# Kernel optimization log

Hardware: AMD Instinct MI355X
Metric: run time of the kernel (lower is better)

## Reference

```python
import jax, jax.numpy as jnp
import numpy as np

# dims derived from config (hidden=512, d_state=64, d_conv=4, expand=2, headdim=64, ngroups=1)
D_MODEL = 512
D_STATE = 64
D_CONV = 4
D_INNER = 2 * D_MODEL          # 1024
HEADDIM = 64
NHEADS = D_INNER // HEADDIM    # 16
CONV_DIM = D_INNER + 2 * D_STATE   # 1152
D_IN_PROJ = 2 * D_INNER + 2 * D_STATE + NHEADS  # 2192
B = 4
L_TOT = 1024                   # seq_len (1008) + puzzle_emb_len (16)
INTER_T = 2816                 # find_multiple(round(4*1024*2/3), 256)
INTER_M = 1536                 # find_multiple(round(4*512*2/3), 256)
EPS = 1e-5


def rms_norm(x, eps=EPS):
    # weightless RMSNorm computed in fp32 (as HRM's rms_norm)
    x32 = x.astype(jnp.float32)
    y = x32 * jax.lax.rsqrt(jnp.mean(x32 * x32, axis=-1, keepdims=True) + eps)
    return y.astype(x.dtype)


def silu(x):
    return x * jax.nn.sigmoid(x)


def swiglu(x, w_gu, w_d):
    gate, up = jnp.split(x @ w_gu.T, 2, axis=-1)
    return (silu(gate) * up) @ w_d.T


def mamba2(u, in_proj_w, conv_w, conv_b, dt_bias, A_log, D, norm_w, out_proj_w):
    b, l, _ = u.shape
    zxbcdt = u @ in_proj_w.T                       # (b, l, D_IN_PROJ)
    z = zxbcdt[..., :D_INNER]
    xBC = zxbcdt[..., D_INNER:D_INNER + CONV_DIM]
    dt = jax.nn.softplus(zxbcdt[..., -NHEADS:] + dt_bias)  # (b, l, H)
    # causal depthwise conv1d over time + SiLU
    xp = jnp.pad(xBC, ((0, 0), (D_CONV - 1, 0), (0, 0)))
    xc = conv_b + sum(xp[:, i:i + l, :] * conv_w[:, i] for i in range(D_CONV))
    xBC = silu(xc)
    x = xBC[..., :D_INNER].reshape(b, l, NHEADS, HEADDIM)      # (b,l,h,p)
    Bm = xBC[..., D_INNER:D_INNER + D_STATE]                    # (b,l,n) ngroups=1
    Cm = xBC[..., D_INNER + D_STATE:]                           # (b,l,n)
    A = -jnp.exp(A_log)                                         # (h,)

    def step(s, inp):
        x_t, B_t, C_t, dt_t = inp                # (b,h,p) (b,n) (b,n) (b,h)
        dA = jnp.exp(dt_t * A)                   # (b,h)
        s = s * dA[:, :, None, None] + (dt_t[:, :, None] * x_t)[..., None] * B_t[:, None, None, :]
        y_t = jnp.einsum('bhpn,bn->bhp', s, C_t)
        return s, y_t

    s0 = jnp.zeros((b, NHEADS, HEADDIM, D_STATE), u.dtype)
    xs = (x.transpose(1, 0, 2, 3), Bm.transpose(1, 0, 2), Cm.transpose(1, 0, 2), dt.transpose(1, 0, 2))
    _, ys = jax.lax.scan(step, s0, xs)
    y = ys.transpose(1, 0, 2, 3) + x * D[None, None, :, None]   # skip term D*x per head
    y = y.reshape(b, l, D_INNER)
    # gated RMSNorm (norm_before_gate=False): norm(y * silu(z)) * weight
    g = y * silu(z)
    g32 = g.astype(jnp.float32)
    g = (g32 * jax.lax.rsqrt(jnp.mean(g32 * g32, axis=-1, keepdims=True) + EPS)).astype(g.dtype) * norm_w
    return g @ out_proj_w.T


def setup_inputs() -> dict:
    key = jax.random.key(0)
    ks = jax.random.split(key, 12)
    s = 0.02
    return {
        'hidden_states': jax.random.normal(ks[0], (B, L_TOT, D_MODEL), jnp.float32),
        'in_proj_w': jax.random.normal(ks[1], (D_IN_PROJ, D_MODEL), jnp.float32) * s,
        'conv_w': jax.random.normal(ks[2], (CONV_DIM, D_CONV), jnp.float32) * 0.1,
        'conv_b': jnp.zeros((CONV_DIM,), jnp.float32),
        'dt_bias': jax.random.normal(ks[3], (NHEADS,), jnp.float32) * 0.5,
        'A_log': jnp.log(jnp.arange(1, NHEADS + 1, dtype=jnp.float32)),
        'D': jnp.ones((NHEADS,), jnp.float32),
        'norm_w': jnp.ones((D_INNER,), jnp.float32),
        'out_proj_w': jax.random.normal(ks[4], (D_MODEL, D_INNER), jnp.float32) * s,
        'gu_t': jax.random.normal(ks[5], (2 * INTER_T, L_TOT), jnp.float32) * s,
        'down_t': jax.random.normal(ks[6], (L_TOT, INTER_T), jnp.float32) * s,
        'gu_m': jax.random.normal(ks[7], (2 * INTER_M, D_MODEL), jnp.float32) * s,
        'down_m': jax.random.normal(ks[8], (D_MODEL, INTER_M), jnp.float32) * s,
    }


def reference(hidden_states, in_proj_w, conv_w, conv_b, dt_bias, A_log, D, norm_w, out_proj_w, gu_t, down_t, gu_m, down_m):
    # Mamba2 mixer -> post-norm
    h = rms_norm(hidden_states + mamba2(hidden_states, in_proj_w, conv_w, conv_b, dt_bias, A_log, D, norm_w, out_proj_w))
    # MLP-t cross mixer over the sequence dim -> post-norm
    x = h.transpose(0, 2, 1)                 # (b, d, L)
    x = rms_norm(x + swiglu(x, gu_t, down_t))
    h = x.transpose(0, 2, 1)
    # token MLP -> post-norm
    h = rms_norm(h + swiglu(h, gu_m, down_m))
    return h
```

## Files before the change

### kernel.cpp

```cpp
#include <hip/hip_runtime.h>


#define BB 4
#define LL 1024
#define DMODEL 512
#define DINNER 1024
#define NHEADS 16
#define HEADDIM 64
#define DSTATE 64
#define CONVDIM 1152
#define NPROJ 2192
#define NPROJ_PAD 2304
#define INTER_T 2816
#define INTER_M 1536
#define NCHUNK 32
#define CHUNK 32

typedef __bf16 bf16x8 __attribute__((ext_vector_type(8)));
typedef float  f32x4  __attribute__((ext_vector_type(4)));
typedef unsigned short u16;
typedef unsigned int   u32;
typedef unsigned short u16x8 __attribute__((ext_vector_type(8)));

__device__ __forceinline__ u16 f2bf(float x) {
    union { float f; u32 u; } v; v.f = x;
    u32 u = v.u;
    return (u16)((u + 0x7fffu + ((u >> 16) & 1u)) >> 16);
}
__device__ __forceinline__ float silu_f(float x) {
    return x / (1.f + __expf(-x));
}
__device__ __forceinline__ float bf2f(u16 w) {
    union { u32 u; float f; } a; a.u = ((u32)w) << 16; return a.f;
}

__device__ __forceinline__ void cstore(float* p, float v) { *p = v; }
__device__ __forceinline__ void cstore(u16*   p, float v) { *p = f2bf(v); }

__device__ __forceinline__ void gld_lds16(const u16* g, u16* l) {
    __builtin_amdgcn_global_load_lds(
        (const __attribute__((address_space(1))) unsigned int*)g,
        (__attribute__((address_space(3))) unsigned int*)l, 16, 0, 0);
}

__device__ __forceinline__ float block_sum(float v) {
    #pragma unroll
    for (int off = 32; off > 0; off >>= 1) v += __shfl_xor(v, off, 64);
    __shared__ float red[4];
    int w = threadIdx.x >> 6;
    int nwv = blockDim.x >> 6;
    if ((threadIdx.x & 63) == 0) red[w] = v;
    __syncthreads();
    float tot = red[0];
    for (int i = 1; i < nwv; i++) tot += red[i];
    return tot;
}

#define HID_E      2097152LL
#define INPROJ_P_E 1179648LL
#define INPROJ_S_E 1122304LL
#define OUTPROJ_E   524288LL
#define GUT_E      5767168LL
#define DOWNT_E    2883584LL
#define GUM_E      1572864LL
#define DOWNM_E     786432LL
#define CONV_TOT_E 14811136LL

__global__ __launch_bounds__(256) void convert_all_kernel(
    const float* __restrict__ s_hid, const float* __restrict__ s_inproj,
    const float* __restrict__ s_outproj, const float* __restrict__ s_gut,
    const float* __restrict__ s_downt, const float* __restrict__ s_gum,
    const float* __restrict__ s_downm, u16* __restrict__ dst)
{
    long long idx = (long long)blockIdx.x * 256 + threadIdx.x;
    long long e = idx * 4;
    if (e >= CONV_TOT_E) return;
    const float* src; long long off, nsrc;
    long long c0 = HID_E;
    long long c1 = c0 + INPROJ_P_E;
    long long c2 = c1 + OUTPROJ_E;
    long long c3 = c2 + GUT_E;
    long long c4 = c3 + DOWNT_E;
    long long c5 = c4 + GUM_E;
    if      (e < c0) { src = s_hid;     off = e;      nsrc = HID_E; }
    else if (e < c1) { src = s_inproj;  off = e - c0; nsrc = INPROJ_S_E; }
    else if (e < c2) { src = s_outproj; off = e - c1; nsrc = OUTPROJ_E; }
    else if (e < c3) { src = s_gut;     off = e - c2; nsrc = GUT_E; }
    else if (e < c4) { src = s_downt;   off = e - c3; nsrc = DOWNT_E; }
    else if (e < c5) { src = s_gum;     off = e - c4; nsrc = GUM_E; }
    else             { src = s_downm;   off = e - c5; nsrc = DOWNM_E; }
    ushort4 r;
    if (off < nsrc) {
        float4 v = *reinterpret_cast<const float4*>(src + off);
        r.x = f2bf(v.x); r.y = f2bf(v.y); r.z = f2bf(v.z); r.w = f2bf(v.w);
    } else {
        r.x = 0; r.y = 0; r.z = 0; r.w = 0;
    }
    *reinterpret_cast<ushort4*>(dst + e) = r;
}

template<bool SK, typename CT>
__device__ __forceinline__ void gemm_bt_body(
    const u16* __restrict__ A, const u16* __restrict__ W,
    CT* __restrict__ C, int M, int N, int K, int kLen)
{
    __shared__ u16 As[128 * 64];
    __shared__ u16 Bs[128 * 64];
    int tid = threadIdx.x;
    int m0 = blockIdx.y * 128, n0 = blockIdx.x * 128;
    int kBase = SK ? blockIdx.z * kLen : 0;
    CT* Cw = SK ? C + (size_t)blockIdx.z * M * N : C;
    int wave = tid >> 6, lane = tid & 63;
    int wm = (wave >> 1) * 64, wn = (wave & 1) * 64;
    int lrow = lane & 15;
    int kq = lane >> 4;
    int kx = lrow & 7;

    int rL = lane >> 3, cL = lane & 7;
    int cG = cL ^ rL;
    const u16* gA[4]; const u16* gB[4];
    u16 *lA[4], *lB[4];
    #pragma unroll
    for (int i = 0; i < 4; i++) {
        int r = wave * 32 + i * 8;
        gA[i] = A + (size_t)(m0 + r + rL) * K + kBase + cG * 8;
        gB[i] = W + (size_t)(n0 + r + rL) * K + kBase + cG * 8;
        lA[i] = &As[r * 64];
        lB[i] = &Bs[r * 64];
    }

    f32x4 acc[4][4];
    #pragma unroll
    for (int i = 0; i < 4; i++)
        #pragma unroll
        for (int j = 0; j < 4; j++) {
            acc[i][j][0] = 0.f; acc[i][j][1] = 0.f;
            acc[i][j][2] = 0.f; acc[i][j][3] = 0.f;
        }

    for (int kt = 0; kt < kLen; kt += 64) {
        __syncthreads();
        #pragma unroll
        for (int i = 0; i < 4; i++) {
            gld_lds16(gA[i] + kt, lA[i]);
            gld_lds16(gB[i] + kt, lB[i]);
        }
        __syncthreads();
        #pragma unroll
        for (int ks = 0; ks < 2; ks++) {
            int ko = (((ks * 4 + kq) ^ kx) * 8);
            bf16x8 af[4], bfr[4];
            #pragma unroll
            for (int i = 0; i < 4; i++) {
                af[i]  = *reinterpret_cast<const bf16x8*>(&As[(wm + i * 16 + lrow) * 64 + ko]);
                bfr[i] = *reinterpret_cast<const bf16x8*>(&Bs[(wn + i * 16 + lrow) * 64 + ko]);
            }
            #pragma unroll
            for (int i = 0; i < 4; i++)
                #pragma unroll
                for (int j = 0; j < 4; j++)
                    acc[i][j] = __builtin_amdgcn_mfma_f32_16x16x32_bf16(af[i], bfr[j], acc[i][j], 0, 0, 0);
        }
    }

    int rbase = m0 + wm + kq * 4;
    int cbase = n0 + wn + lrow;
    #pragma unroll
    for (int i = 0; i < 4; i++)
        #pragma unroll
        for (int j = 0; j < 4; j++)
            #pragma unroll
            for (int r = 0; r < 4; r++)
                cstore(&Cw[(size_t)(rbase + i * 16 + r) * N + cbase + j * 16], acc[i][j][r]);
}

__global__ __launch_bounds__(256) void gemm_bt(
    const u16* __restrict__ A, const u16* __restrict__ W,
    u16* __restrict__ C, int M, int N, int K)
{
    gemm_bt_body<false, u16>(A, W, C, M, N, K, K);
}

__global__ __launch_bounds__(256) void gemm_bt_sk(
    const u16* __restrict__ A, const u16* __restrict__ W,
    u16* __restrict__ C, int M, int N, int K, int kLen)
{
    gemm_bt_body<true, u16>(A, W, C, M, N, K, kLen);
}

__global__ __launch_bounds__(256) void gemm_swiglu(
    const u16* __restrict__ A, const u16* __restrict__ W,
    u16* __restrict__ act, int M, int inter, int K)
{
    __shared__ u16 As[128 * 64];
    __shared__ u16 Bs[128 * 64];
    int tid = threadIdx.x;
    int m0 = blockIdx.y * 128, n0 = blockIdx.x * 64;
    int wave = tid >> 6, lane = tid & 63;
    int wm = (wave >> 1) * 64, wn = (wave & 1) * 32;
    int lrow = lane & 15;
    int kq = lane >> 4;
    int kx = lrow & 7;

    int rL = lane >> 3, cL = lane & 7;
    int cG = cL ^ rL;
    const u16* gA[4]; const u16* gB[4];
    u16 *lA[4], *lB[4];
    #pragma unroll
    for (int i = 0; i < 4; i++) {
        int r = wave * 32 + i * 8;
        gA[i] = A + (size_t)(m0 + r + rL) * K + cG * 8;
        lA[i] = &As[r * 64];
        int rB = r;
        int grow = (rB < 64) ? (n0 + rB + rL)
                             : (inter + n0 + rB - 64 + rL);
        gB[i] = W + (size_t)grow * K + cG * 8;
        lB[i] = &Bs[rB * 64];
    }

    f32x4 accg[4][2], accu[4][2];
    #pragma unroll
    for (int i = 0; i < 4; i++)
        #pragma unroll
        for (int j = 0; j < 2; j++) {
            accg[i][j][0]=0.f; accg[i][j][1]=0.f; accg[i][j][2]=0.f; accg[i][j][3]=0.f;
            accu[i][j][0]=0.f; accu[i][j][1]=0.f; accu[i][j][2]=0.f; accu[i][j][3]=0.f;
        }

    for (int kt = 0; kt < K; kt += 64) {
        __syncthreads();
        #pragma unroll
        for (int i = 0; i < 4; i++) {
            gld_lds16(gA[i] + kt, lA[i]);
            gld_lds16(gB[i] + kt, lB[i]);
        }
        __syncthreads();
        #pragma unroll
        for (int ks = 0; ks < 2; ks++) {
            int ko = (((ks * 4 + kq) ^ kx) * 8);
            bf16x8 af[4], bg[2], bu[2];
            #pragma unroll
            for (int i = 0; i < 4; i++)
                af[i] = *reinterpret_cast<const bf16x8*>(&As[(wm + i * 16 + lrow) * 64 + ko]);
            #pragma unroll
            for (int j = 0; j < 2; j++) {
                bg[j] = *reinterpret_cast<const bf16x8*>(&Bs[(wn + j * 16 + lrow) * 64 + ko]);
                bu[j] = *reinterpret_cast<const bf16x8*>(&Bs[(64 + wn + j * 16 + lrow) * 64 + ko]);
            }
            #pragma unroll
            for (int i = 0; i < 4; i++)
                #pragma unroll
                for (int j = 0; j < 2; j++) {
                    accg[i][j] = __builtin_amdgcn_mfma_f32_16x16x32_bf16(af[i], bg[j], accg[i][j], 0, 0, 0);
                    accu[i][j] = __builtin_amdgcn_mfma_f32_16x16x32_bf16(af[i], bu[j], accu[i][j], 0, 0, 0);
                }
        }
    }

    int rbase = m0 + wm + kq * 4;
    int cbase = n0 + wn + lrow;
    #pragma unroll
    for (int i = 0; i < 4; i++)
        #pragma unroll
        for (int j = 0; j < 2; j++)
            #pragma unroll
            for (int r = 0; r < 4; r++) {
                float g = accg[i][j][r], u = accu[i][j][r];
                act[(size_t)(rbase + i * 16 + r) * inter + cbase + j * 16] =
                    f2bf(silu_f(g) * u);
            }
}

__global__ __launch_bounds__(256) void conv_dt_kernel(
    const u16* __restrict__ zx, const float* __restrict__ conv_w,
    const float* __restrict__ conv_b, const float* __restrict__ dt_bias,
    u16* __restrict__ convout, float* __restrict__ dtbuf)
{
    int idx = blockIdx.x * 256 + threadIdx.x;
    int bl = idx / 1168;
    int c  = idx - bl * 1168;
    int l  = bl & (LL - 1);
    if (c < CONVDIM) {
        const u16* col = zx + (size_t)bl * NPROJ_PAD + DINNER + c;
        float acc = conv_b[c];
        #pragma unroll
        for (int i = 0; i < 4; i++) {
            int lt = l - 3 + i;
            float v = (lt >= 0) ? bf2f(col[(long long)(lt - l) * NPROJ_PAD]) : 0.f;
            acc = fmaf(v, conv_w[c * 4 + i], acc);
        }
        convout[(size_t)bl * CONVDIM + c] = f2bf(silu_f(acc));
    } else {
        int h = c - CONVDIM;
        float v = bf2f(zx[(size_t)bl * NPROJ_PAD + 2176 + h]) + dt_bias[h];
        float sp = (v > 20.f) ? v : log1pf(__expf(v));
        dtbuf[(size_t)bl * NHEADS + h] = sp;
    }
}

__global__ __launch_bounds__(256) void scan_mfma1(
    const u16* __restrict__ convout, const float* __restrict__ dtbuf,
    const float* __restrict__ A_log, u16* __restrict__ Sc,
    float* __restrict__ Ptot, u16* __restrict__ yp0)
{
    __shared__ u16 Blds[32 * 72];
    __shared__ u16 Clds[32 * 72];
    __shared__ u16 Xt[4][64 * 40];
    __shared__ u16 Bht[4][64 * 40];
    __shared__ u16 Wlds[4][32 * 40];
    __shared__ float dtl[4][32], cuml[4][32], warr[4][32];

    int blk = blockIdx.x;
    int c   = blk & 31;
    int bg  = blk >> 5;
    int b   = bg >> 2;
    int hq  = bg & 3;
    int tid = threadIdx.x;
    int w    = tid >> 6;
    int lane = tid & 63;
    int h   = hq * 4 + w;
    int bh  = b * 16 + h;
    int lrow = lane & 15, kq = lane >> 4;
    size_t base = ((size_t)b * LL + (size_t)c * CHUNK) * CONVDIM;
    float Ah = -__expf(A_log[h]);

    if (lane < 32)
        dtl[w][lane] = dtbuf[((size_t)b * LL + (size_t)c * CHUNK + lane) * NHEADS + h];
    #pragma unroll
    for (int it = 0; it < 2; ++it) {
        int idx = it * 256 + tid;
        int t = idx >> 4, q = idx & 15;
        u16x8 v = *reinterpret_cast<const u16x8*>(
            &convout[base + (size_t)t * CONVDIM + DINNER + q * 8]);
        if (q < 8) *reinterpret_cast<u16x8*>(&Blds[t * 72 + q * 8]) = v;
        else       *reinterpret_cast<u16x8*>(&Clds[t * 72 + (q - 8) * 8]) = v;
    }
    #pragma unroll
    for (int t = 0; t < 32; ++t)
        Xt[w][lane * 40 + t] = convout[base + (size_t)t * CONVDIM + h * HEADDIM + lane];
    __syncthreads();

    float s_inc = 0.f, s_all = 0.f;
    #pragma unroll
    for (int j = 0; j < 32; ++j) {
        float v = dtl[w][j];
        s_all += v;
        if (j <= lane) s_inc += v;
    }
    if (lane < 32) {
        cuml[w][lane] = s_inc;
        warr[w][lane] = __expf(Ah * (s_all - s_inc)) * dtl[w][lane];
    }
    float cumTot = s_all;
    __syncthreads();

    #pragma unroll
    for (int t = 0; t < 32; ++t)
        Bht[w][lane * 40 + t] = f2bf(warr[w][t] * bf2f(Blds[t * 72 + lane]));

    f32x4 accG[2][2];
    #pragma unroll
    for (int i = 0; i < 2; i++)
        #pragma unroll
        for (int j = 0; j < 2; j++) {
            accG[i][j][0]=0.f; accG[i][j][1]=0.f; accG[i][j][2]=0.f; accG[i][j][3]=0.f;
        }
    #pragma unroll
    for (int ks = 0; ks < 2; ++ks) {
        bf16x8 af[2], bfr[2];
        #pragma unroll
        for (int i = 0; i < 2; i++) {
            af[i]  = *reinterpret_cast<const bf16x8*>(&Clds[(16*i + lrow) * 72 + ks*32 + kq*8]);
            bfr[i] = *reinterpret_cast<const bf16x8*>(&Blds[(16*i + lrow) * 72 + ks*32 + kq*8]);
        }
        #pragma unroll
        for (int i = 0; i < 2; i++)
            #pragma unroll
            for (int j = 0; j < 2; j++)
                accG[i][j] = __builtin_amdgcn_mfma_f32_16x16x32_bf16(af[i], bfr[j], accG[i][j], 0, 0, 0);
    }

    float ctp0 = cuml[w][lrow],      dtp0 = dtl[w][lrow];
    float ctp1 = cuml[w][16 + lrow], dtp1 = dtl[w][16 + lrow];
    #pragma unroll
    for (int i = 0; i < 2; i++)
        #pragma unroll
        for (int r = 0; r < 4; r++) {
            int t = 16*i + kq*4 + r;
            float ct = cuml[w][t];
            #pragma unroll
            for (int j = 0; j < 2; j++) {
                int tp = 16*j + lrow;
                float ctp = j ? ctp1 : ctp0;
                float dtp = j ? dtp1 : dtp0;
                float g = accG[i][j][r];
                float wv = (tp <= t) ? __expf(Ah * (ct - ctp)) * dtp * g : 0.f;
                Wlds[w][t * 40 + tp] = f2bf(wv);
            }
        }
    __syncthreads();

    bf16x8 xf[4];
    #pragma unroll
    for (int j = 0; j < 4; j++)
        xf[j] = *reinterpret_cast<const bf16x8*>(&Xt[w][(16*j + lrow) * 40 + kq*8]);
    f32x4 accY[2][4];
    #pragma unroll
    for (int i = 0; i < 2; i++) {
        bf16x8 wf = *reinterpret_cast<const bf16x8*>(&Wlds[w][(16*i + lrow) * 40 + kq*8]);
        #pragma unroll
        for (int j = 0; j < 4; j++) {
            accY[i][j][0]=0.f; accY[i][j][1]=0.f; accY[i][j][2]=0.f; accY[i][j][3]=0.f;
            accY[i][j] = __builtin_amdgcn_mfma_f32_16x16x32_bf16(wf, xf[j], accY[i][j], 0, 0, 0);
        }
    }

    f32x4 accS[4][4];
    #pragma unroll
    for (int j = 0; j < 4; j++) {
        bf16x8 bb = *reinterpret_cast<const bf16x8*>(&Bht[w][(16*j + lrow) * 40 + kq*8]);
        #pragma unroll
        for (int i = 0; i < 4; i++) {
            accS[i][j][0]=0.f; accS[i][j][1]=0.f; accS[i][j][2]=0.f; accS[i][j][3]=0.f;
            accS[i][j] = __builtin_amdgcn_mfma_f32_16x16x32_bf16(xf[i], bb, accS[i][j], 0, 0, 0);
        }
    }

    u16* yb = yp0 + ((size_t)b * LL + (size_t)c * CHUNK) * DINNER + h * HEADDIM;
    #pragma unroll
    for (int i = 0; i < 2; i++)
        #pragma unroll
        for (int r = 0; r < 4; r++) {
            int t = 16*i + kq*4 + r;
            #pragma unroll
            for (int j = 0; j < 4; j++)
                yb[(size_t)t * DINNER + 16*j + lrow] = f2bf(accY[i][j][r]);
        }
    #pragma unroll
    for (int i = 0; i < 4; i++)
        #pragma unroll
        for (int r = 0; r < 4; r++) {
            int p = 16*i + kq*4 + r;
            #pragma unroll
            for (int j = 0; j < 4; j++)
                Sc[((size_t)(bh * 4 + j) * NCHUNK + c) * 1024 + p * 16 + lrow] = f2bf(accS[i][j][r]);
        }
    if (lane == 0) Ptot[bh * NCHUNK + c] = __expf(Ah * cumTot);
}

__global__ __launch_bounds__(256) void scan_combine(
    const u16* __restrict__ Sc, const float* __restrict__ Ptot,
    u16* __restrict__ Sinit)
{
    int blk = blockIdx.x;
    int bh = blk >> 2;
    int tid = threadIdx.x;
    int p = tid >> 2;
    int ncol = (tid & 3) * 4;
    float Pv[NCHUNK];
    #pragma unroll
    for (int c = 0; c < NCHUNK; ++c) Pv[c] = Ptot[bh * NCHUNK + c];
    float4 carry; carry.x = 0.f; carry.y = 0.f; carry.z = 0.f; carry.w = 0.f;
    size_t rowbase = (size_t)blk * NCHUNK * 1024 + p * 16 + ncol;
    #pragma unroll
    for (int c = 0; c < NCHUNK; ++c) {
        size_t row = rowbase + (size_t)c * 1024;
        ushort4 o;
        o.x = f2bf(carry.x); o.y = f2bf(carry.y);
        o.z = f2bf(carry.z); o.w = f2bf(carry.w);
        *reinterpret_cast<ushort4*>(Sinit + row) = o;
        ushort4 si = *reinterpret_cast<const ushort4*>(Sc + row);
        carry.x = fmaf(carry.x, Pv[c], bf2f(si.x));
        carry.y = fmaf(carry.y, Pv[c], bf2f(si.y));
        carry.z = fmaf(carry.z, Pv[c], bf2f(si.z));
        carry.w = fmaf(carry.w, Pv[c], bf2f(si.w));
    }
}

__global__ __launch_bounds__(256) void scan_mfma2(
    const u16* __restrict__ convout, const float* __restrict__ dtbuf,
    const float* __restrict__ A_log, const u16* __restrict__ Sinit,
    u16* __restrict__ yp1)
{
    __shared__ u16 Clds2[32 * 72];
    __shared__ float dtl[4][32], dacl[4][32];
    int blk = blockIdx.x;
    int c   = blk & 31;
    int bg  = blk >> 5;
    int b   = bg >> 2;
    int hq  = bg & 3;
    int tid = threadIdx.x;
    int w    = tid >> 6;
    int lane = tid & 63;
    int h   = hq * 4 + w;
    int bh  = b * 16 + h;
    int lrow = lane & 15, kq = lane >> 4;
    size_t base = ((size_t)b * LL + (size_t)c * CHUNK) * CONVDIM;
    float Ah = -__expf(A_log[h]);

    if (lane < 32)
        dtl[w][lane] = dtbuf[((size_t)b * LL + (size_t)c * CHUNK + lane) * NHEADS + h];
    {
        int t = tid >> 3, q = tid & 7;
        u16x8 v = *reinterpret_cast<const u16x8*>(
            &convout[base + (size_t)t * CONVDIM + DINNER + DSTATE + q * 8]);
        *reinterpret_cast<u16x8*>(&Clds2[t * 72 + q * 8]) = v;
    }
    __syncthreads();

    float s_inc = 0.f;
    #pragma unroll
    for (int j = 0; j < 32; ++j) {
        float v = dtl[w][j];
        if (j <= lane) s_inc += v;
    }
    if (lane < 32) dacl[w][lane] = __expf(Ah * s_inc);

    f32x4 accI[2][4];
    #pragma unroll
    for (int i = 0; i < 2; i++)
        #pragma unroll
        for (int j = 0; j < 4; j++) {
            accI[i][j][0]=0.f; accI[i][j][1]=0.f; accI[i][j][2]=0.f; accI[i][j][3]=0.f;
        }
    #pragma unroll
    for (int ks = 0; ks < 2; ++ks) {
        bf16x8 ca[2];
        #pragma unroll
        for (int i = 0; i < 2; i++)
            ca[i] = *reinterpret_cast<const bf16x8*>(&Clds2[(16*i + lrow) * 72 + ks*32 + kq*8]);
        int nq = ks * 2 + (kq >> 1);
        int off = (kq & 1) * 8;
        #pragma unroll
        for (int j = 0; j < 4; j++) {
            int p = 16*j + lrow;
            const u16* sp = Sinit + ((size_t)(bh * 4 + nq) * NCHUNK + c) * 1024 + p * 16 + off;
            bf16x8 fr = *reinterpret_cast<const bf16x8*>(sp);
            #pragma unroll
            for (int i = 0; i < 2; i++)
                accI[i][j] = __builtin_amdgcn_mfma_f32_16x16x32_bf16(ca[i], fr, accI[i][j], 0, 0, 0);
        }
    }

    u16* yb = yp1 + ((size_t)b * LL + (size_t)c * CHUNK) * DINNER + h * HEADDIM;
    #pragma unroll
    for (int i = 0; i < 2; i++)
        #pragma unroll
        for (int r = 0; r < 4; r++) {
            int t = 16*i + kq*4 + r;
            float sct = dacl[w][t];
            #pragma unroll
            for (int j = 0; j < 4; j++)
                yb[(size_t)t * DINNER + 16*j + lrow] = f2bf(accI[i][j][r] * sct);
        }
}

__global__ __launch_bounds__(256) void gated_rms_kernel(
    const u16* __restrict__ yp0, const u16* __restrict__ yp1,
    const u16* __restrict__ convout, const u16* __restrict__ zx,
    const float* __restrict__ Dv, const float* __restrict__ norm_w,
    u16* __restrict__ gout)
{
    int bl = blockIdx.x;
    int c = threadIdx.x * 4;
    ushort4 y0 = *reinterpret_cast<const ushort4*>(yp0 + (size_t)bl * DINNER + c);
    ushort4 y1 = *reinterpret_cast<const ushort4*>(yp1 + (size_t)bl * DINNER + c);
    ushort4 xv = *reinterpret_cast<const ushort4*>(convout + (size_t)bl * CONVDIM + c);
    ushort4 zv = *reinterpret_cast<const ushort4*>(zx + (size_t)bl * NPROJ_PAD + c);
    float Dh = Dv[c >> 6];
    float g0 = (bf2f(y0.x) + bf2f(y1.x) + bf2f(xv.x) * Dh) * silu_f(bf2f(zv.x));
    float g1 = (bf2f(y0.y) + bf2f(y1.y) + bf2f(xv.y) * Dh) * silu_f(bf2f(zv.y));
    float g2 = (bf2f(y0.z) + bf2f(y1.z) + bf2f(xv.z) * Dh) * silu_f(bf2f(zv.z));
    float g3 = (bf2f(y0.w) + bf2f(y1.w) + bf2f(xv.w) * Dh) * silu_f(bf2f(zv.w));
    float tot = block_sum(g0 * g0 + g1 * g1 + g2 * g2 + g3 * g3);
    float sc = rsqrtf(tot * (1.f / DINNER) + 1e-5f);
    float4 nw = *reinterpret_cast<const float4*>(norm_w + c);
    ushort4 o;
    o.x = f2bf(g0 * sc * nw.x); o.y = f2bf(g1 * sc * nw.y);
    o.z = f2bf(g2 * sc * nw.z); o.w = f2bf(g3 * sc * nw.w);
    *reinterpret_cast<ushort4*>(gout + (size_t)bl * DINNER + c) = o;
}

template<typename AT, typename OT>
__device__ __forceinline__ void residual_rms_body(
    const AT* __restrict__ a, const u16* __restrict__ pbuf,
    OT* __restrict__ outf, int ncols, int rows)
{
    int row = blockIdx.x;
    int c = threadIdx.x * 4;
    size_t slice = (size_t)rows * ncols;
    size_t off = (size_t)row * ncols + c;
    float va0, va1, va2, va3;
    if constexpr (sizeof(AT) == 4) {
        float4 t = *reinterpret_cast<const float4*>((const float*)a + off);
        va0 = t.x; va1 = t.y; va2 = t.z; va3 = t.w;
    } else {
        ushort4 t = *reinterpret_cast<const ushort4*>((const u16*)a + off);
        va0 = bf2f(t.x); va1 = bf2f(t.y); va2 = bf2f(t.z); va3 = bf2f(t.w);
    }
    ushort4 p0 = *reinterpret_cast<const ushort4*>(pbuf + off);
    ushort4 p1 = *reinterpret_cast<const ushort4*>(pbuf + slice + off);
    ushort4 p2 = *reinterpret_cast<const ushort4*>(pbuf + 2 * slice + off);
    ushort4 p3 = *reinterpret_cast<const ushort4*>(pbuf + 3 * slice + off);
    float v0 = va0 + ((bf2f(p0.x) + bf2f(p1.x)) + (bf2f(p2.x) + bf2f(p3.x)));
    float v1 = va1 + ((bf2f(p0.y) + bf2f(p1.y)) + (bf2f(p2.y) + bf2f(p3.y)));
    float v2 = va2 + ((bf2f(p0.z) + bf2f(p1.z)) + (bf2f(p2.z) + bf2f(p3.z)));
    float v3 = va3 + ((bf2f(p0.w) + bf2f(p1.w)) + (bf2f(p2.w) + bf2f(p3.w)));
    float tot = block_sum(v0 * v0 + v1 * v1 + v2 * v2 + v3 * v3);
    float sc = rsqrtf(tot / (float)ncols + 1e-5f);
    if constexpr (sizeof(OT) == 4) {
        float4 o; o.x = v0 * sc; o.y = v1 * sc; o.z = v2 * sc; o.w = v3 * sc;
        *reinterpret_cast<float4*>((float*)outf + off) = o;
    } else {
        ushort4 o;
        o.x = f2bf(v0 * sc); o.y = f2bf(v1 * sc);
        o.z = f2bf(v2 * sc); o.w = f2bf(v3 * sc);
        *reinterpret_cast<ushort4*>((u16*)outf + off) = o;
    }
}

__global__ void residual_rms_f2b(const float* __restrict__ a,
    const u16* __restrict__ pbuf, u16* __restrict__ o, int ncols, int rows)
{ residual_rms_body<float, u16>(a, pbuf, o, ncols, rows); }

__global__ void residual_rms_b2b(const u16* __restrict__ a,
    const u16* __restrict__ pbuf, u16* __restrict__ o, int ncols, int rows)
{ residual_rms_body<u16, u16>(a, pbuf, o, ncols, rows); }

__global__ void residual_rms_b2f(const u16* __restrict__ a,
    const u16* __restrict__ pbuf, float* __restrict__ o, int ncols, int rows)
{ residual_rms_body<u16, float>(a, pbuf, o, ncols, rows); }

__global__ __launch_bounds__(256) void transpose_bf16_kernel(
    const u16* __restrict__ in, u16* __restrict__ outb, int R, int C)
{
    __shared__ u16 tile[32][34];
    int b = blockIdx.z;
    int c0 = blockIdx.x * 32, r0 = blockIdx.y * 32;
    const u16* ip = in + (size_t)b * R * C;
    for (int i = threadIdx.y; i < 32; i += 8)
        tile[i][threadIdx.x] = ip[(size_t)(r0 + i) * C + c0 + threadIdx.x];
    __syncthreads();
    size_t ob = (size_t)b * R * C;
    for (int i = threadIdx.y; i < 32; i += 8)
        outb[ob + (size_t)(c0 + i) * R + r0 + threadIdx.x] = tile[threadIdx.x][i];
}

extern "C" void kernel_launch(void* const* d_in, const int* in_sizes, int n_in,
                              void* d_out, int out_size, void* d_ws, size_t ws_size,
                              hipStream_t stream)
{
    const float* hid      = (const float*)d_in[0];
    const float* in_proj  = (const float*)d_in[1];
    const float* conv_w   = (const float*)d_in[2];
    const float* conv_b   = (const float*)d_in[3];
    const float* dt_bias  = (const float*)d_in[4];
    const float* A_log    = (const float*)d_in[5];
    const float* Dv       = (const float*)d_in[6];
    const float* norm_w   = (const float*)d_in[7];
    const float* out_proj = (const float*)d_in[8];
    const float* gu_t     = (const float*)d_in[9];
    const float* down_t   = (const float*)d_in[10];
    const float* gu_m     = (const float*)d_in[11];
    const float* down_m   = (const float*)d_in[12];
    float* outp = (float*)d_out;

    char* ws = (char*)d_ws;
    u16* bf        = (u16*)ws;
    u16* hid_bf    = bf;
    u16* w_inproj  = bf + HID_E;
    u16* w_outproj = w_inproj + INPROJ_P_E;
    u16* w_gut     = w_outproj + OUTPROJ_E;
    u16* w_downt   = w_gut + GUT_E;
    u16* w_gum     = w_downt + DOWNT_E;
    u16* w_downm   = w_gum + GUM_E;
    size_t o = (size_t)(CONV_TOT_E * 2);
    auto alloc = [&](size_t bytes) { size_t r = o; o = (o + bytes + 255) & ~(size_t)255; return r; };
    size_t dt_off  = alloc(4096 * 16 * 4);
    size_t g_off   = alloc((size_t)4096 * 1024 * 2);
    size_t h1_off  = alloc((size_t)4096 * 512 * 4);
    size_t Pt_off  = alloc(2048 * 4);
    size_t xtb_off = alloc((size_t)2048 * 1024 * 2);
    size_t xtf_off = alloc((size_t)2048 * 1024 * 4);
    size_t act1_off= alloc((size_t)2048 * 2816 * 2);
    size_t x2_off  = alloc((size_t)2048 * 1024 * 4);
    size_t h2b_off = alloc((size_t)4096 * 512 * 2);
    size_t h2f_off = alloc((size_t)4096 * 512 * 4);
    size_t act2_off= alloc((size_t)4096 * 1536 * 2);
    size_t pad_off = alloc((size_t)10 * 1024 * 1024);
    size_t Sc_off  = xtb_off;
    size_t Si_off  = xtb_off + (size_t)8192 * 1024 * 4;
    (void)pad_off; (void)xtf_off; (void)h2f_off;
    size_t R_off   = o;
    size_t zx_off  = R_off;
    size_t cv_off  = zx_off + (size_t)4096 * NPROJ_PAD * 4;
    size_t y_off   = cv_off + (size_t)4096 * CONVDIM * 4;
    size_t sk_off  = R_off;

    u16*   zx      = (u16*)(ws + zx_off);
    u16*   convout = (u16*)(ws + cv_off);
    u16*   ybuf    = (u16*)(ws + y_off);
    float* dtbuf   = (float*)(ws + dt_off);
    u16*   g_bf    = (u16*)(ws + g_off);
    u16*   h1_bf   = (u16*)(ws + h1_off);
    u16*   xt_bf   = (u16*)(ws + xtb_off);
    u16*   act1    = (u16*)(ws + act1_off);
    u16*   x2_bf   = (u16*)(ws + x2_off);
    u16*   h2_bf   = (u16*)(ws + h2b_off);
    u16*   act2    = (u16*)(ws + act2_off);
    u16*   skbuf   = (u16*)(ws + sk_off);
    u16*   Sc      = (u16*)(ws + Sc_off);
    u16*   Sinit   = (u16*)(ws + Si_off);
    float* Ptot    = (float*)(ws + Pt_off);

    convert_all_kernel<<<14464, 256, 0, stream>>>(
        hid, in_proj, out_proj, gu_t, down_t, gu_m, down_m, bf);

    gemm_bt<<<dim3(NPROJ_PAD / 128, 4096 / 128), 256, 0, stream>>>(
        hid_bf, w_inproj, zx, 4096, NPROJ_PAD, 512);

    conv_dt_kernel<<<18688, 256, 0, stream>>>(zx, conv_w, conv_b, dt_bias, convout, dtbuf);

    scan_mfma1<<<512, 256, 0, stream>>>(convout, dtbuf, A_log, Sc, Ptot, ybuf);
    scan_combine<<<256, 256, 0, stream>>>(Sc, Ptot, Sinit);
    scan_mfma2<<<512, 256, 0, stream>>>(convout, dtbuf, A_log, Sinit, Sc);

    gated_rms_kernel<<<4096, 256, 0, stream>>>(ybuf, Sc, convout, zx, Dv, norm_w, g_bf);

    gemm_bt_sk<<<dim3(512 / 128, 4096 / 128, 4), 256, 0, stream>>>(
        g_bf, w_outproj, skbuf, 4096, 512, 1024, 256);

    residual_rms_f2b<<<4096, 128, 0, stream>>>(hid, skbuf, h1_bf, 512, 4096);

    transpose_bf16_kernel<<<dim3(16, 32, 4), dim3(32, 8), 0, stream>>>(h1_bf, xt_bf, 1024, 512);

    gemm_swiglu<<<dim3(INTER_T / 64, 2048 / 128), 256, 0, stream>>>(
        xt_bf, w_gut, act1, 2048, INTER_T, 1024);

    gemm_bt_sk<<<dim3(1024 / 128, 2048 / 128, 4), 256, 0, stream>>>(
        act1, w_downt, skbuf, 2048, 1024, 2816, 704);

    residual_rms_b2b<<<2048, 256, 0, stream>>>(xt_bf, skbuf, x2_bf, 1024, 2048);

    transpose_bf16_kernel<<<dim3(32, 16, 4), dim3(32, 8), 0, stream>>>(x2_bf, h2_bf, 512, 1024);

    gemm_swiglu<<<dim3(INTER_M / 64, 4096 / 128), 256, 0, stream>>>(
        h2_bf, w_gum, act2, 4096, INTER_M, 512);

    gemm_bt_sk<<<dim3(512 / 128, 4096 / 128, 4), 256, 0, stream>>>(
        act2, w_downm, skbuf, 4096, 512, 1536, 384);

    residual_rms_b2f<<<4096, 128, 0, stream>>>(h2_bf, skbuf, outp, 512, 4096);
}
```

Baseline: 308.8 us.

## Add XCD-aware block swizzle to GEMMs and split scan_combine across more blocks

Remaps GEMM workgroup indices so that consecutive output tiles land on the same XCD on MI355X, which should improve L2 reuse of the shared A/B tiles. Separately, scan_combine now uses 512 blocks, each thread handling two elements instead of four, to expose more parallelism in the serial chunk-carry loop. The swizzle adds a little index arithmetic per block. The combine change halves the work per thread and uses narrower 4-byte accesses.

```diff
diff --git a/kernel.cpp b/kernel.cpp
--- a/kernel.cpp
+++ b/kernel.cpp
@@ -36,6 +36,17 @@
 
 __device__ __forceinline__ void cstore(float* p, float v) { *p = v; }
 __device__ __forceinline__ void cstore(u16*   p, float v) { *p = f2bf(v); }
+
+__device__ __forceinline__ void xcd_swizzle(int& bx, int& by) {
+    int gx = gridDim.x;
+    int nwg = gx * gridDim.y;
+    int orig = by * gx + bx;
+    int q = nwg >> 3, rr = nwg & 7;
+    int xcd = orig & 7, lid = orig >> 3;
+    int swz = (xcd < rr ? xcd * (q + 1) : rr * (q + 1) + (xcd - rr) * q) + lid;
+    bx = swz % gx;
+    by = swz / gx;
+}
 
 __device__ __forceinline__ void gld_lds16(const u16* g, u16* l) {
     __builtin_amdgcn_global_load_lds(
@@ -107,7 +118,9 @@
     __shared__ u16 As[128 * 64];
     __shared__ u16 Bs[128 * 64];
     int tid = threadIdx.x;
-    int m0 = blockIdx.y * 128, n0 = blockIdx.x * 128;
+    int bx = blockIdx.x, by = blockIdx.y;
+    xcd_swizzle(bx, by);
+    int m0 = by * 128, n0 = bx * 128;
     int kBase = SK ? blockIdx.z * kLen : 0;
     CT* Cw = SK ? C + (size_t)blockIdx.z * M * N : C;
     int wave = tid >> 6, lane = tid & 63;
@@ -195,7 +208,9 @@
     __shared__ u16 As[128 * 64];
     __shared__ u16 Bs[128 * 64];
     int tid = threadIdx.x;
-    int m0 = blockIdx.y * 128, n0 = blockIdx.x * 64;
+    int bx = blockIdx.x, by = blockIdx.y;
+    xcd_swizzle(bx, by);
+    int m0 = by * 128, n0 = bx * 64;
     int wave = tid >> 6, lane = tid & 63;
     int wm = (wave >> 1) * 64, wn = (wave & 1) * 32;
     int lrow = lane & 15;
@@ -453,27 +468,24 @@
     u16* __restrict__ Sinit)
 {
     int blk = blockIdx.x;
-    int bh = blk >> 2;
+    int rowid = blk >> 1;
+    int bh = rowid >> 2;
+    int half = blk & 1;
     int tid = threadIdx.x;
-    int p = tid >> 2;
-    int ncol = (tid & 3) * 4;
+    int e = half * 512 + tid * 2;
     float Pv[NCHUNK];
     #pragma unroll
     for (int c = 0; c < NCHUNK; ++c) Pv[c] = Ptot[bh * NCHUNK + c];
-    float4 carry; carry.x = 0.f; carry.y = 0.f; carry.z = 0.f; carry.w = 0.f;
-    size_t rowbase = (size_t)blk * NCHUNK * 1024 + p * 16 + ncol;
+    float c0v = 0.f, c1v = 0.f;
+    size_t rowbase = (size_t)rowid * NCHUNK * 1024 + e;
     #pragma unroll
     for (int c = 0; c < NCHUNK; ++c) {
         size_t row = rowbase + (size_t)c * 1024;
-        ushort4 o;
-        o.x = f2bf(carry.x); o.y = f2bf(carry.y);
-        o.z = f2bf(carry.z); o.w = f2bf(carry.w);
-        *reinterpret_cast<ushort4*>(Sinit + row) = o;
-        ushort4 si = *reinterpret_cast<const ushort4*>(Sc + row);
-        carry.x = fmaf(carry.x, Pv[c], bf2f(si.x));
-        carry.y = fmaf(carry.y, Pv[c], bf2f(si.y));
-        carry.z = fmaf(carry.z, Pv[c], bf2f(si.z));
-        carry.w = fmaf(carry.w, Pv[c], bf2f(si.w));
+        ushort2 o; o.x = f2bf(c0v); o.y = f2bf(c1v);
+        *reinterpret_cast<ushort2*>(Sinit + row) = o;
+        ushort2 si = *reinterpret_cast<const ushort2*>(Sc + row);
+        c0v = fmaf(c0v, Pv[c], bf2f(si.x));
+        c1v = fmaf(c1v, Pv[c], bf2f(si.y));
     }
 }
 
@@ -722,7 +734,7 @@
     conv_dt_kernel<<<18688, 256, 0, stream>>>(zx, conv_w, conv_b, dt_bias, convout, dtbuf);
 
     scan_mfma1<<<512, 256, 0, stream>>>(convout, dtbuf, A_log, Sc, Ptot, ybuf);
-    scan_combine<<<256, 256, 0, stream>>>(Sc, Ptot, Sinit);
+    scan_combine<<<512, 256, 0, stream>>>(Sc, Ptot, Sinit);
     scan_mfma2<<<512, 256, 0, stream>>>(convout, dtbuf, A_log, Sinit, Sc);
 
     gated_rms_kernel<<<4096, 256, 0, stream>>>(ybuf, Sc, convout, zx, Dv, norm_w, g_bf);
```

New measurement: 305.2 us. About the same (-1.1%).
